# Optimization experiments

Hardware: AMD Instinct MI355X
Metric: run time of the kernel (lower is better)

## Reference

```python
import jax, jax.numpy as jnp
import numpy as np

GF = 25  # gauss_filter_dim

def _gauss(std):
    n = np.arange(GF) - (GF - 1) / 2.0
    return np.exp(-0.5 * (n / std) ** 2).astype(np.float32)

def _ln(x, g, b, eps=1e-5):
    m = jnp.mean(x, -1, keepdims=True)
    v = jnp.mean((x - m) ** 2, -1, keepdims=True)
    return (x - m) * jax.lax.rsqrt(v + eps) * g + b

def _prelu(x, a):
    return jnp.where(x >= 0, x, a * x)

def _lrelu(x, s):
    return jnp.where(x >= 0, x, s * x)

B, D, H, NB = 32768, 128, 256, 4
C = 32  # 2**5

def setup_inputs() -> dict:
    key = jax.random.key(0)
    ks = jax.random.split(key, 16)
    rn = lambda k, s, sc=0.05: (jax.random.normal(k, s, dtype=jnp.float32) * sc)
    filters = jnp.asarray(np.stack([_gauss(0.5), _gauss(1.0), _gauss(3.0)]))  # [3,25]
    return {
        'x': jax.random.normal(ks[0], (B, D), dtype=jnp.float32),
        'filters': filters,
        'W1': rn(ks[1], (H, D)), 'b1': jnp.zeros((H,), jnp.float32),
        'a0': jnp.float32(0.25),  # PReLU scalar
        'g0': jnp.ones((H,), jnp.float32), 'be0': jnp.zeros((H,), jnp.float32),
        'Wc1': rn(ks[2], (NB, C, H)), 'bc1': jnp.zeros((NB, C), jnp.float32),
        'Wc2': rn(ks[3], (NB, C, H)), 'bc2': jnp.zeros((NB, C), jnp.float32),
        'Wc3': rn(ks[4], (NB, C, H)), 'bc3': jnp.zeros((NB, C), jnp.float32),
        'Wcat': rn(ks[5], (NB, H, 3 * C)), 'bcat': jnp.zeros((NB, H), jnp.float32),
        'g1': jnp.ones((NB, H), jnp.float32), 'be1': jnp.zeros((NB, H), jnp.float32),
        'Wf1': rn(ks[6], (NB, H, H)), 'bf1': jnp.zeros((NB, H), jnp.float32),
        'af': jnp.full((NB,), 0.25, jnp.float32),
        'Wf2': rn(ks[7], (NB, H, H)), 'bf2': jnp.zeros((NB, H), jnp.float32),
        'g2': jnp.ones((NB, H), jnp.float32), 'be2': jnp.zeros((NB, H), jnp.float32),
        'Wout': rn(ks[8], (1, H)), 'bout': jnp.zeros((1,), jnp.float32),
    }

def reference(x, filters, W1, b1, a0, g0, be0, Wc1, bc1, Wc2, bc2, Wc3, bc3,
              Wcat, bcat, g1, be1, Wf1, bf1, af, Wf2, bf2, g2, be2, Wout, bout):
    out = _prelu(x @ W1.T + b1, a0)
    out = _ln(out, g0, be0)
    kern = filters[:, None, :]  # [3, 1, GF] -> 3 output channels, 1 input channel
    nb = Wc1.shape[0]
    for i in range(nb):
        res = out
        # batched 'same' 1D conv with the three Gaussian filters in one call: [B,3,H]
        conv = jax.lax.conv_general_dilated(out[:, None, :], kern, (1,), 'SAME')
        x1 = _lrelu(conv[:, 0] @ Wc1[i].T + bc1[i], 0.1)
        x2 = _lrelu(conv[:, 1] @ Wc2[i].T + bc2[i], 0.1)
        x3 = _lrelu(conv[:, 2] @ Wc3[i].T + bc3[i], 0.1)
        out = jnp.concatenate([x1, x2, x3], axis=1) @ Wcat[i].T + bcat[i]
        out = _ln(out + res, g1[i], be1[i])
        res = out
        h = _prelu(out @ Wf1[i].T + bf1[i], af[i])  # dropout inactive (eval)
        h = h @ Wf2[i].T + bf2[i]
        out = _ln(h + res, g2[i], be2[i])
    return out @ Wout.T + bout
```

## Files before the change

### kernel.cpp

```cpp
#include <hip/hip_runtime.h>

typedef __attribute__((ext_vector_type(8))) short bf16x8;
typedef __attribute__((ext_vector_type(4))) float f32x4;

__device__ __forceinline__ float bf2f(unsigned short u) {
    union { unsigned u; float f; } x; x.u = (unsigned)u << 16; return x.f;
}
__device__ __forceinline__ unsigned short f2bf(float f) {
    union { float f; unsigned u; } x; x.f = f;
    unsigned r = x.u + 0x7fffu + ((x.u >> 16) & 1u);
    return (unsigned short)(r >> 16);
}

__global__ __launch_bounds__(256) void prep(
    const float* __restrict__ filters,
    const float* __restrict__ Wc1, const float* __restrict__ Wc2, const float* __restrict__ Wc3,
    const float* __restrict__ bc1, const float* __restrict__ bc2, const float* __restrict__ bc3,
    const float* __restrict__ W1, const float* __restrict__ Wcat,
    const float* __restrict__ Wf1, const float* __restrict__ Wf2,
    unsigned short* __restrict__ W1b, unsigned short* __restrict__ wceffb,
    float* __restrict__ bceff, unsigned short* __restrict__ Wcatb,
    unsigned short* __restrict__ Wf1b, unsigned short* __restrict__ Wf2b)
{
    int idx = blockIdx.x * 256 + threadIdx.x;
    if (idx < 65536) {
        int n = idx >> 8, k = idx & 255;
        W1b[idx] = (k < 128) ? f2bf(W1[n * 128 + k]) : (unsigned short)0;
    } else if (idx < 196608) {
        int j = idx - 65536;
        int i = j >> 15, n = (j >> 8) & 127, h = j & 255;
        if (n < 96) {
            int c = n >> 5, jj = n & 31;
            const float* Wc = (c == 0) ? Wc1 : (c == 1) ? Wc2 : Wc3;
            const float* f  = filters + c * 25;
            float acc = 0.f;
            #pragma unroll
            for (int k = 0; k < 25; ++k) {
                int hh = h + 12 - k;
                if (hh >= 0 && hh < 256) acc += f[k] * Wc[(i * 32 + jj) * 256 + hh];
            }
            wceffb[j] = f2bf(acc);
            if (h == 0) {
                const float* bc = (c == 0) ? bc1 : (c == 1) ? bc2 : bc3;
                bceff[i * 128 + n] = bc[i * 32 + jj];
            }
        } else {
            wceffb[j] = 0;
            if (h == 0) bceff[i * 128 + n] = 0.f;
        }
    } else if (idx < 458752) {
        int j = idx - 196608;
        int i = j >> 16, rem = j & 65535, n = rem >> 8, k = rem & 255;
        Wcatb[j] = (k < 96) ? f2bf(Wcat[(i * 256 + n) * 96 + k]) : (unsigned short)0;
    } else if (idx < 720896) {
        int j = idx - 458752;
        Wf1b[j] = f2bf(Wf1[j]);
    } else if (idx < 983040) {
        int j = idx - 720896;
        Wf2b[j] = f2bf(Wf2[j]);
    }
}

template<int NKC, int NWT>
__device__ __forceinline__ void gemm_stage(
    const unsigned short* __restrict__ Wg,
    const float* __restrict__ bias,
    const unsigned short* actIn, unsigned short* actOut,
    float* scratch,
    int actmode, const float* alphap,
    const unsigned short* resbuf,
    const float* g, const float* be,
    int finaldot, const float* Wout, const float* boutp, float* outg, int rowbase)
{
    const int tid  = threadIdx.x;
    const int lane = tid & 63;
    const int wave = tid >> 6;
    const int wm   = wave >> 2;
    const int wn   = wave & 3;
    const int l15  = lane & 15;
    const int hi   = lane >> 4;

    f32x4 acc[4][NWT];
    #pragma unroll
    for (int mt = 0; mt < 4; ++mt)
        #pragma unroll
        for (int nt = 0; nt < NWT; ++nt) acc[mt][nt] = (f32x4){0.f, 0.f, 0.f, 0.f};

    const unsigned short* wbase = Wg + ((size_t)(wn * NWT) * 16 + l15) * 256 + hi * 8;
    const unsigned short* abase = actIn + (wm * 4) * 8 * 512 + lane * 8;

    bf16x8 w0[NWT], w1[NWT], a0[4], a1[4];

    #define LOADW(dst, kc) { _Pragma("unroll") \
        for (int nt = 0; nt < NWT; ++nt) \
            dst[nt] = *(const bf16x8*)(wbase + nt * 16 * 256 + (kc) * 32); }
    #define LOADA(dst, kc) { _Pragma("unroll") \
        for (int mt = 0; mt < 4; ++mt) \
            dst[mt] = *(const bf16x8*)(abase + (mt * 8 + (kc)) * 512); }
    #define FMAS(areg, wreg) { \
        __builtin_amdgcn_s_setprio(1); \
        _Pragma("unroll") \
        for (int mt = 0; mt < 4; ++mt) { _Pragma("unroll") \
            for (int nt = 0; nt < NWT; ++nt) \
                acc[mt][nt] = __builtin_amdgcn_mfma_f32_16x16x32_bf16( \
                    wreg[nt], areg[mt], acc[mt][nt], 0, 0, 0); } \
        __builtin_amdgcn_s_setprio(0); }

    LOADW(w0, 0); LOADA(a0, 0);
    #pragma unroll
    for (int kc = 0; kc < NKC; kc += 2) {
        if (kc + 1 < NKC) { LOADW(w1, kc + 1); LOADA(a1, kc + 1); }
        FMAS(a0, w0);
        if (kc + 2 < NKC) { LOADW(w0, kc + 2); LOADA(a0, kc + 2); }
        if (kc + 1 < NKC) FMAS(a1, w1);
    }
    #undef LOADW
    #undef LOADA
    #undef FMAS

    const float alpha = alphap ? alphap[0] : 0.1f;
    float vv[4][NWT][4];
    #pragma unroll
    for (int mt = 0; mt < 4; ++mt) {
        #pragma unroll
        for (int nt = 0; nt < NWT; ++nt) {
            const int nb = wn * (NWT * 16) + nt * 16 + hi * 4;
            const float4 bs = *(const float4*)(bias + nb);
            float t0 = acc[mt][nt][0] + bs.x;
            float t1 = acc[mt][nt][1] + bs.y;
            float t2 = acc[mt][nt][2] + bs.z;
            float t3 = acc[mt][nt][3] + bs.w;
            if (actmode) {
                t0 = t0 >= 0.f ? t0 : alpha * t0;
                t1 = t1 >= 0.f ? t1 : alpha * t1;
                t2 = t2 >= 0.f ? t2 : alpha * t2;
                t3 = t3 >= 0.f ? t3 : alpha * t3;
            }
            if (resbuf) {
                const int ro = ((wm * 4 + mt) * 8 + (nb >> 5)) * 512
                             + (l15 + ((nb >> 3) & 3) * 16) * 8 + (nb & 7);
                const ushort4 rv = *(const ushort4*)(resbuf + ro);
                t0 += bf2f(rv.x); t1 += bf2f(rv.y); t2 += bf2f(rv.z); t3 += bf2f(rv.w);
            }
            vv[mt][nt][0] = t0; vv[mt][nt][1] = t1;
            vv[mt][nt][2] = t2; vv[mt][nt][3] = t3;
        }
    }

    float* lnred = scratch;
    float mean[4], rstd[4];
    if (g) {
        #pragma unroll
        for (int mt = 0; mt < 4; ++mt) {
            float s = 0.f, q = 0.f;
            #pragma unroll
            for (int nt = 0; nt < NWT; ++nt)
                #pragma unroll
                for (int r = 0; r < 4; ++r) { const float v = vv[mt][nt][r]; s += v; q += v * v; }
            s += __shfl_xor(s, 16); s += __shfl_xor(s, 32);
            q += __shfl_xor(q, 16); q += __shfl_xor(q, 32);
            if (hi == 0)
                *(float2*)(lnred + (wm * 64 + mt * 16 + l15) * 8 + wn * 2) = make_float2(s, q);
        }
        __syncthreads();
        #pragma unroll
        for (int mt = 0; mt < 4; ++mt) {
            const int m = wm * 64 + mt * 16 + l15;
            const float4 p0 = *(const float4*)(lnred + m * 8);
            const float4 p1 = *(const float4*)(lnred + m * 8 + 4);
            const float s = p0.x + p0.z + p1.x + p1.z;
            const float q = p0.y + p0.w + p1.y + p1.w;
            const float mu = s * (1.f / 256.f);
            mean[mt] = mu;
            rstd[mt] = rsqrtf(q * (1.f / 256.f) - mu * mu + 1e-5f);
        }
    }

    float* dotp = scratch + 1024;
    #pragma unroll
    for (int mt = 0; mt < 4; ++mt) {
        float dp = 0.f;
        #pragma unroll
        for (int nt = 0; nt < NWT; ++nt) {
            const int nb = wn * (NWT * 16) + nt * 16 + hi * 4;
            float o0 = vv[mt][nt][0], o1 = vv[mt][nt][1], o2 = vv[mt][nt][2], o3 = vv[mt][nt][3];
            if (g) {
                const float4 gv = *(const float4*)(g + nb);
                const float4 bv = *(const float4*)(be + nb);
                o0 = (o0 - mean[mt]) * rstd[mt] * gv.x + bv.x;
                o1 = (o1 - mean[mt]) * rstd[mt] * gv.y + bv.y;
                o2 = (o2 - mean[mt]) * rstd[mt] * gv.z + bv.z;
                o3 = (o3 - mean[mt]) * rstd[mt] * gv.w + bv.w;
            }
            if (!finaldot) {
                const ushort4 ov = {f2bf(o0), f2bf(o1), f2bf(o2), f2bf(o3)};
                *(ushort4*)(actOut + ((wm * 4 + mt) * 8 + (nb >> 5)) * 512
                            + (l15 + ((nb >> 3) & 3) * 16) * 8 + (nb & 7)) = ov;
            } else {
                const float4 wv = *(const float4*)(Wout + nb);
                dp += o0 * wv.x + o1 * wv.y + o2 * wv.z + o3 * wv.w;
            }
        }
        if (finaldot) {
            dp += __shfl_xor(dp, 16); dp += __shfl_xor(dp, 32);
            if (hi == 0) dotp[(wm * 64 + mt * 16 + l15) * 4 + wn] = dp;
        }
    }
    if (finaldot) {
        __syncthreads();
        if (tid < 128) {
            const float4 pp = *(const float4*)(dotp + tid * 4);
            outg[rowbase + tid] = pp.x + pp.y + pp.z + pp.w + boutp[0];
        }
    }
    __syncthreads();
}

__global__ __launch_bounds__(512, 2) void mega(
    const float* __restrict__ x,
    const unsigned short* __restrict__ W1b, const float* __restrict__ b1,
    const float* __restrict__ a0, const float* __restrict__ g0, const float* __restrict__ be0,
    const unsigned short* __restrict__ wceffb, const float* __restrict__ bceff,
    const unsigned short* __restrict__ Wcatb, const float* __restrict__ bcat,
    const float* __restrict__ g1, const float* __restrict__ be1,
    const unsigned short* __restrict__ Wf1b, const float* __restrict__ bf1,
    const float* __restrict__ af,
    const unsigned short* __restrict__ Wf2b, const float* __restrict__ bf2,
    const float* __restrict__ g2, const float* __restrict__ be2,
    const float* __restrict__ Wout, const float* __restrict__ boutp,
    float* __restrict__ outg)
{
    __shared__ __align__(16) unsigned short actA[32768];
    __shared__ __align__(16) unsigned short actB[32768];
    __shared__ __align__(16) float scratch[1536];

    const int tid = threadIdx.x;
    const int rowbase = blockIdx.x * 128;

    {
        const int r = tid >> 2, q = tid & 3;
        const float* xp = x + (size_t)(rowbase + r) * 128 + q * 32;
        #pragma unroll
        for (int gi = 0; gi < 8; ++gi) {
            const float4 xv = *(const float4*)(xp + gi * 4);
            const int j = q * 32 + gi * 4;
            const ushort4 o = {f2bf(xv.x), f2bf(xv.y), f2bf(xv.z), f2bf(xv.w)};
            *(ushort4*)(actB + ((r >> 4) * 8 + (j >> 5)) * 512
                        + ((r & 15) + ((j >> 3) & 3) * 16) * 8 + (j & 7)) = o;
        }
        __syncthreads();
    }

    gemm_stage<4, 4>(W1b, b1, actB, actA, scratch, 1, a0, nullptr, g0, be0,
                     0, nullptr, nullptr, nullptr, 0);

    for (int it = 0; it < 4; ++it) {
        gemm_stage<8, 2>(wceffb + it * 32768, bceff + it * 128, actA, actB, scratch,
                         2, nullptr, nullptr, nullptr, nullptr,
                         0, nullptr, nullptr, nullptr, 0);
        gemm_stage<4, 4>(Wcatb + it * 65536, bcat + it * 256, actB, actA, scratch,
                         0, nullptr, actA, g1 + it * 256, be1 + it * 256,
                         0, nullptr, nullptr, nullptr, 0);
        gemm_stage<8, 4>(Wf1b + it * 65536, bf1 + it * 256, actA, actB, scratch,
                         1, af + it, nullptr, nullptr, nullptr,
                         0, nullptr, nullptr, nullptr, 0);
        gemm_stage<8, 4>(Wf2b + it * 65536, bf2 + it * 256, actB, actA, scratch,
                         0, nullptr, actA, g2 + it * 256, be2 + it * 256,
                         (it == 3) ? 1 : 0, Wout, boutp, outg, rowbase);
    }
}

extern "C" void kernel_launch(void* const* d_in, const int* in_sizes, int n_in,
                              void* d_out, int out_size, void* d_ws, size_t ws_size,
                              hipStream_t stream)
{
    const float* x       = (const float*)d_in[0];
    const float* filters = (const float*)d_in[1];
    const float* W1      = (const float*)d_in[2];
    const float* b1      = (const float*)d_in[3];
    const float* a0      = (const float*)d_in[4];
    const float* g0      = (const float*)d_in[5];
    const float* be0     = (const float*)d_in[6];
    const float* Wc1     = (const float*)d_in[7];
    const float* bc1     = (const float*)d_in[8];
    const float* Wc2     = (const float*)d_in[9];
    const float* bc2     = (const float*)d_in[10];
    const float* Wc3     = (const float*)d_in[11];
    const float* bc3     = (const float*)d_in[12];
    const float* Wcat    = (const float*)d_in[13];
    const float* bcat    = (const float*)d_in[14];
    const float* g1      = (const float*)d_in[15];
    const float* be1     = (const float*)d_in[16];
    const float* Wf1     = (const float*)d_in[17];
    const float* bf1     = (const float*)d_in[18];
    const float* af      = (const float*)d_in[19];
    const float* Wf2     = (const float*)d_in[20];
    const float* bf2     = (const float*)d_in[21];
    const float* g2      = (const float*)d_in[22];
    const float* be2     = (const float*)d_in[23];
    const float* Wout    = (const float*)d_in[24];
    const float* boutp   = (const float*)d_in[25];
    float* outf = (float*)d_out;

    unsigned short* p = (unsigned short*)d_ws;
    unsigned short* W1b    = p;
    unsigned short* wceffb = p + 65536;
    unsigned short* Wcatb  = p + 196608;
    unsigned short* Wf1b   = p + 458752;
    unsigned short* Wf2b   = p + 720896;
    float*          bceff  = (float*)(p + 983040);

    prep<<<dim3(3840), dim3(256), 0, stream>>>(
        filters, Wc1, Wc2, Wc3, bc1, bc2, bc3, W1, Wcat, Wf1, Wf2,
        W1b, wceffb, bceff, Wcatb, Wf1b, Wf2b);

    mega<<<dim3(256), dim3(512), 0, stream>>>(
        x, W1b, b1, a0, g0, be0, wceffb, bceff, Wcatb, bcat, g1, be1,
        Wf1b, bf1, af, Wf2b, bf2, g2, be2, Wout, boutp, outf);
}
```

Before: 158.1 us.

## Shrink mega-kernel row tile to 32 rows with 256-thread blocks

Each block of the fused MLP kernel now handles 32 rows with 4 waves instead of 128 rows with 8 waves. The launch grows from 256 to 1024 blocks, and LDS per block drops to a single activation buffer plus one scratch buffer, with the first stage written in place. The aim is more resident waves per CU to hide memory and MFMA latency. In exchange, every block re-reads the full weight set from L2, so total weight traffic is four times higher, and each loaded weight fragment feeds half as many MFMAs.

```diff
diff --git a/kernel.cpp b/kernel.cpp
--- a/kernel.cpp
+++ b/kernel.cpp
@@ -66,7 +66,8 @@
     const unsigned short* __restrict__ Wg,
     const float* __restrict__ bias,
     const unsigned short* actIn, unsigned short* actOut,
-    float* scratch,
+    float* lnred,
+    float* dotp,
     int actmode, const float* alphap,
     const unsigned short* resbuf,
     const float* g, const float* be,
@@ -74,33 +75,31 @@
 {
     const int tid  = threadIdx.x;
     const int lane = tid & 63;
-    const int wave = tid >> 6;
-    const int wm   = wave >> 2;
-    const int wn   = wave & 3;
+    const int wn   = tid >> 6;
     const int l15  = lane & 15;
     const int hi   = lane >> 4;
 
-    f32x4 acc[4][NWT];
+    f32x4 acc[2][NWT];
     #pragma unroll
-    for (int mt = 0; mt < 4; ++mt)
+    for (int mt = 0; mt < 2; ++mt)
         #pragma unroll
         for (int nt = 0; nt < NWT; ++nt) acc[mt][nt] = (f32x4){0.f, 0.f, 0.f, 0.f};
 
     const unsigned short* wbase = Wg + ((size_t)(wn * NWT) * 16 + l15) * 256 + hi * 8;
-    const unsigned short* abase = actIn + (wm * 4) * 8 * 512 + lane * 8;
-
-    bf16x8 w0[NWT], w1[NWT], a0[4], a1[4];
+    const unsigned short* abase = actIn + lane * 8;
+
+    bf16x8 w0[NWT], w1[NWT], a0[2], a1[2];
 
     #define LOADW(dst, kc) { _Pragma("unroll") \
         for (int nt = 0; nt < NWT; ++nt) \
             dst[nt] = *(const bf16x8*)(wbase + nt * 16 * 256 + (kc) * 32); }
     #define LOADA(dst, kc) { _Pragma("unroll") \
-        for (int mt = 0; mt < 4; ++mt) \
+        for (int mt = 0; mt < 2; ++mt) \
             dst[mt] = *(const bf16x8*)(abase + (mt * 8 + (kc)) * 512); }
     #define FMAS(areg, wreg) { \
         __builtin_amdgcn_s_setprio(1); \
         _Pragma("unroll") \
-        for (int mt = 0; mt < 4; ++mt) { _Pragma("unroll") \
+        for (int mt = 0; mt < 2; ++mt) { _Pragma("unroll") \
             for (int nt = 0; nt < NWT; ++nt) \
                 acc[mt][nt] = __builtin_amdgcn_mfma_f32_16x16x32_bf16( \
                     wreg[nt], areg[mt], acc[mt][nt], 0, 0, 0); } \
@@ -119,9 +118,9 @@
     #undef FMAS
 
     const float alpha = alphap ? alphap[0] : 0.1f;
-    float vv[4][NWT][4];
+    float vv[2][NWT][4];
     #pragma unroll
-    for (int mt = 0; mt < 4; ++mt) {
+    for (int mt = 0; mt < 2; ++mt) {
         #pragma unroll
         for (int nt = 0; nt < NWT; ++nt) {
             const int nb = wn * (NWT * 16) + nt * 16 + hi * 4;
@@ -137,7 +136,7 @@
                 t3 = t3 >= 0.f ? t3 : alpha * t3;
             }
             if (resbuf) {
-                const int ro = ((wm * 4 + mt) * 8 + (nb >> 5)) * 512
+                const int ro = (mt * 8 + (nb >> 5)) * 512
                              + (l15 + ((nb >> 3) & 3) * 16) * 8 + (nb & 7);
                 const ushort4 rv = *(const ushort4*)(resbuf + ro);
                 t0 += bf2f(rv.x); t1 += bf2f(rv.y); t2 += bf2f(rv.z); t3 += bf2f(rv.w);
@@ -147,11 +146,10 @@
         }
     }
 
-    float* lnred = scratch;
-    float mean[4], rstd[4];
+    float mean[2], rstd[2];
     if (g) {
         #pragma unroll
-        for (int mt = 0; mt < 4; ++mt) {
+        for (int mt = 0; mt < 2; ++mt) {
             float s = 0.f, q = 0.f;
             #pragma unroll
             for (int nt = 0; nt < NWT; ++nt)
@@ -160,12 +158,12 @@
             s += __shfl_xor(s, 16); s += __shfl_xor(s, 32);
             q += __shfl_xor(q, 16); q += __shfl_xor(q, 32);
             if (hi == 0)
-                *(float2*)(lnred + (wm * 64 + mt * 16 + l15) * 8 + wn * 2) = make_float2(s, q);
+                *(float2*)(lnred + (mt * 16 + l15) * 8 + wn * 2) = make_float2(s, q);
         }
         __syncthreads();
         #pragma unroll
-        for (int mt = 0; mt < 4; ++mt) {
-            const int m = wm * 64 + mt * 16 + l15;
+        for (int mt = 0; mt < 2; ++mt) {
+            const int m = mt * 16 + l15;
             const float4 p0 = *(const float4*)(lnred + m * 8);
             const float4 p1 = *(const float4*)(lnred + m * 8 + 4);
             const float s = p0.x + p0.z + p1.x + p1.z;
@@ -176,9 +174,8 @@
         }
     }
 
-    float* dotp = scratch + 1024;
     #pragma unroll
-    for (int mt = 0; mt < 4; ++mt) {
+    for (int mt = 0; mt < 2; ++mt) {
         float dp = 0.f;
         #pragma unroll
         for (int nt = 0; nt < NWT; ++nt) {
@@ -194,7 +191,7 @@
             }
             if (!finaldot) {
                 const ushort4 ov = {f2bf(o0), f2bf(o1), f2bf(o2), f2bf(o3)};
-                *(ushort4*)(actOut + ((wm * 4 + mt) * 8 + (nb >> 5)) * 512
+                *(ushort4*)(actOut + (mt * 8 + (nb >> 5)) * 512
                             + (l15 + ((nb >> 3) & 3) * 16) * 8 + (nb & 7)) = ov;
             } else {
                 const float4 wv = *(const float4*)(Wout + nb);
@@ -203,12 +200,12 @@
         }
         if (finaldot) {
             dp += __shfl_xor(dp, 16); dp += __shfl_xor(dp, 32);
-            if (hi == 0) dotp[(wm * 64 + mt * 16 + l15) * 4 + wn] = dp;
+            if (hi == 0) dotp[(mt * 16 + l15) * 4 + wn] = dp;
         }
     }
     if (finaldot) {
         __syncthreads();
-        if (tid < 128) {
+        if (tid < 32) {
             const float4 pp = *(const float4*)(dotp + tid * 4);
             outg[rowbase + tid] = pp.x + pp.y + pp.z + pp.w + boutp[0];
         }
@@ -216,7 +213,7 @@
     __syncthreads();
 }
 
-__global__ __launch_bounds__(512, 2) void mega(
+__global__ __launch_bounds__(256, 4) void mega(
     const float* __restrict__ x,
     const unsigned short* __restrict__ W1b, const float* __restrict__ b1,
     const float* __restrict__ a0, const float* __restrict__ g0, const float* __restrict__ be0,
@@ -230,42 +227,43 @@
     const float* __restrict__ Wout, const float* __restrict__ boutp,
     float* __restrict__ outg)
 {
-    __shared__ __align__(16) unsigned short actA[32768];
-    __shared__ __align__(16) unsigned short actB[32768];
-    __shared__ __align__(16) float scratch[1536];
+    __shared__ __align__(16) unsigned short act[8192];
+    __shared__ __align__(16) unsigned short hbuf[8192];
+    __shared__ __align__(16) float lnred[256];
 
     const int tid = threadIdx.x;
-    const int rowbase = blockIdx.x * 128;
+    const int rowbase = blockIdx.x * 32;
+    float* dotp = (float*)hbuf;
 
     {
-        const int r = tid >> 2, q = tid & 3;
-        const float* xp = x + (size_t)(rowbase + r) * 128 + q * 32;
-        #pragma unroll
-        for (int gi = 0; gi < 8; ++gi) {
+        const int r = tid >> 3, q = tid & 7;
+        const float* xp = x + (size_t)(rowbase + r) * 128 + q * 16;
+        #pragma unroll
+        for (int gi = 0; gi < 4; ++gi) {
             const float4 xv = *(const float4*)(xp + gi * 4);
-            const int j = q * 32 + gi * 4;
+            const int j = q * 16 + gi * 4;
             const ushort4 o = {f2bf(xv.x), f2bf(xv.y), f2bf(xv.z), f2bf(xv.w)};
-            *(ushort4*)(actB + ((r >> 4) * 8 + (j >> 5)) * 512
+            *(ushort4*)(act + ((r >> 4) * 8 + (j >> 5)) * 512
                         + ((r & 15) + ((j >> 3) & 3) * 16) * 8 + (j & 7)) = o;
         }
         __syncthreads();
     }
 
-    gemm_stage<4, 4>(W1b, b1, actB, actA, scratch, 1, a0, nullptr, g0, be0,
+    gemm_stage<4, 4>(W1b, b1, act, act, lnred, dotp, 1, a0, nullptr, g0, be0,
                      0, nullptr, nullptr, nullptr, 0);
 
     for (int it = 0; it < 4; ++it) {
-        gemm_stage<8, 2>(wceffb + it * 32768, bceff + it * 128, actA, actB, scratch,
+        gemm_stage<8, 2>(wceffb + it * 32768, bceff + it * 128, act, hbuf, lnred, dotp,
                          2, nullptr, nullptr, nullptr, nullptr,
                          0, nullptr, nullptr, nullptr, 0);
-        gemm_stage<4, 4>(Wcatb + it * 65536, bcat + it * 256, actB, actA, scratch,
-                         0, nullptr, actA, g1 + it * 256, be1 + it * 256,
+        gemm_stage<4, 4>(Wcatb + it * 65536, bcat + it * 256, hbuf, act, lnred, dotp,
+                         0, nullptr, act, g1 + it * 256, be1 + it * 256,
                          0, nullptr, nullptr, nullptr, 0);
-        gemm_stage<8, 4>(Wf1b + it * 65536, bf1 + it * 256, actA, actB, scratch,
+        gemm_stage<8, 4>(Wf1b + it * 65536, bf1 + it * 256, act, hbuf, lnred, dotp,
                          1, af + it, nullptr, nullptr, nullptr,
                          0, nullptr, nullptr, nullptr, 0);
-        gemm_stage<8, 4>(Wf2b + it * 65536, bf2 + it * 256, actB, actA, scratch,
-                         0, nullptr, actA, g2 + it * 256, be2 + it * 256,
+        gemm_stage<8, 4>(Wf2b + it * 65536, bf2 + it * 256, hbuf, act, lnred, dotp,
+                         0, nullptr, act, g2 + it * 256, be2 + it * 256,
                          (it == 3) ? 1 : 0, Wout, boutp, outg, rowbase);
     }
 }
@@ -314,7 +312,7 @@
         filters, Wc1, Wc2, Wc3, bc1, bc2, bc3, W1, Wcat, Wf1, Wf2,
         W1b, wceffb, bceff, Wcatb, Wf1b, Wf2b);
 
-    mega<<<dim3(256), dim3(512), 0, stream>>>(
+    mega<<<dim3(1024), dim3(256), 0, stream>>>(
         x, W1b, b1, a0, g0, be0, wceffb, bceff, Wcatb, bcat, g1, be1,
         Wf1b, bf1, af, Wf2b, bf2, g2, be2, Wout, boutp, outf);
 }
```

After: 223.2 us. 1.41x slower.
